# Performance work log

Measured on AMD Instinct MI355X. Metric: run time of the kernel, lower is better.

Reference implementation:

```python
import jax, jax.numpy as jnp
import numpy as np

B, S, H = 4, 2048, 2048
FFN, E, TOP_K = 5632, 8, 2

def setup_inputs() -> dict:
    key = jax.random.key(0)
    k1, k2, k3, k4, k5 = jax.random.split(key, 5)
    return {
        "hidden_states": jax.random.normal(k1, (B, S, H), dtype=jnp.float32),
        "wg": jax.random.normal(k2, (H, E), dtype=jnp.float32) * 0.02,
        "wg_ema": jnp.zeros((H, E), dtype=jnp.float32),
        "fc1_1": jax.random.normal(k3, (E, FFN, H), dtype=jnp.float32) * 0.02,
        "fc1_2": jax.random.normal(k4, (E, FFN, H), dtype=jnp.float32) * 0.02,
        "fc2": jax.random.normal(k5, (E, H, FFN), dtype=jnp.float32) * 0.02,
    }

def reference(hidden_states, wg, wg_ema, fc1_1, fc1_2, fc2):
    b, s, h = hidden_states.shape
    x = hidden_states.reshape(-1, h)  # [T, H]
    # Router: P6TopkCapGate mixes the live gate with its EMA 50/50.
    wg_running = 0.5 * (wg_ema + wg.astype(jnp.float32))
    router_logits = x.astype(jnp.float32) @ wg_running  # [T, E]
    probs = jax.nn.softmax(router_logits, axis=-1)
    top_vals, top_idx = jax.lax.top_k(probs, TOP_K)  # [T, K]
    routing_weights = (top_vals / top_vals.sum(axis=-1, keepdims=True)).astype(x.dtype)
    out = jnp.zeros_like(x)
    n_experts = fc1_1.shape[0]
    for e in range(n_experts):
        # combine weight per token for this expert (0 if not routed here)
        w_e = jnp.sum(routing_weights * (top_idx == e), axis=-1)  # [T]
        h1 = x @ fc1_1[e].T            # [T, FFN]
        h2 = x @ fc1_2[e].T            # [T, FFN]
        y = (jax.nn.silu(h1) * h2) @ fc2[e].T  # [T, H]
        out = out + w_e[:, None] * y
    return out.reshape(b, s, h), router_logits
```

## Files before the change

### kernel.cpp

```cpp
#include <hip/hip_runtime.h>
#include <stdint.h>

#define TT 8192
#define HD 2048
#define FFN 5632
#define NE 8
#define NPK 11264

typedef float f32x4 __attribute__((ext_vector_type(4)));
typedef _Float16 f16x8 __attribute__((ext_vector_type(8)));
typedef unsigned int u32;

#define OFF_WR    0ul
#define OFF_CNT   65536ul
#define OFF_LISTS 66048ul
#define OFF_TOKW  328192ul
#define OFF_ACT   1048576ul
#define OFF_XH    (OFF_ACT + 184549376ul)
#define OFF_WPK   (OFF_XH + 33554432ul)
#define OFF_W3H   OFF_WPK

__device__ __forceinline__ void gl_lds16(const void* g, void* s) {
  __builtin_amdgcn_global_load_lds((const __attribute__((address_space(1))) u32*)g,
                                   (__attribute__((address_space(3))) u32*)s, 16, 0, 0);
}

#define VM4() asm volatile("s_waitcnt vmcnt(4)" ::: "memory")
#define VM0() asm volatile("s_waitcnt vmcnt(0)" ::: "memory")

__device__ __forceinline__ f16x8 cvt8(f32x4 a, f32x4 b) {
  f16x8 r;
  r[0] = (_Float16)a[0]; r[1] = (_Float16)a[1]; r[2] = (_Float16)a[2]; r[3] = (_Float16)a[3];
  r[4] = (_Float16)b[0]; r[5] = (_Float16)b[1]; r[6] = (_Float16)b[2]; r[7] = (_Float16)b[3];
  return r;
}

__global__ __launch_bounds__(256) void k_cvt(const float* __restrict__ in,
                                             _Float16* __restrict__ out, long n8) {
  long i = (long)blockIdx.x * 256 + threadIdx.x;
  const long stride = (long)gridDim.x * 256;
  for (; i < n8; i += stride) {
    f32x4 a = ((const f32x4*)in)[i * 2];
    f32x4 b = ((const f32x4*)in)[i * 2 + 1];
    ((f16x8*)out)[i] = cvt8(a, b);
  }
}

__global__ __launch_bounds__(256) void k_cvtpack(const float* __restrict__ fc11,
                                                 const float* __restrict__ fc12,
                                                 _Float16* __restrict__ wpk) {
  const long total = (long)NE * NPK * 256;
  long i8 = (long)blockIdx.x * 256 + threadIdx.x;
  const long stride = (long)gridDim.x * 256;
  for (; i8 < total; i8 += stride) {
    int k8 = (int)(i8 & 255);
    long qe = i8 >> 8;
    int q = (int)(qe % NPK);
    int e = (int)(qe / NPK);
    int c = q & 255;
    int f = (q >> 8) * 128 + ((c >> 6) & 3) * 32 + ((c >> 4) & 1) * 16 + (c & 15);
    const float* src = ((c >> 5) & 1 ? fc12 : fc11) + ((size_t)e * FFN + f) * HD + k8 * 8;
    f32x4 a = *(const f32x4*)src;
    f32x4 b = *(const f32x4*)(src + 4);
    *(f16x8*)(wpk + qe * HD + (size_t)k8 * 8) = cvt8(a, b);
  }
}

__global__ __launch_bounds__(256) void k_prep(const float* __restrict__ wg,
                                              const float* __restrict__ wge,
                                              float* __restrict__ wr) {
  int i = blockIdx.x * 256 + threadIdx.x;
  if (i < HD * NE) wr[i] = 0.5f * (wge[i] + wg[i]);
}

__global__ __launch_bounds__(256) void k_router(const float* __restrict__ x,
                                                const float* __restrict__ wr,
                                                float* __restrict__ logits,
                                                float* __restrict__ tokw,
                                                int* __restrict__ lists,
                                                int* __restrict__ cnt,
                                                _Float16* __restrict__ xh) {
  const int t = blockIdx.x, tid = threadIdx.x;
  const float* xr = x + (size_t)t * HD;
  _Float16* xo = xh + (size_t)t * HD;
  float acc[NE];
#pragma unroll
  for (int e = 0; e < NE; ++e) acc[e] = 0.f;
  for (int h = tid; h < HD; h += 256) {
    float xv = xr[h];
    xo[h] = (_Float16)xv;
    const float* w = wr + h * NE;
#pragma unroll
    for (int e = 0; e < NE; ++e) acc[e] = fmaf(xv, w[e], acc[e]);
  }
#pragma unroll
  for (int e = 0; e < NE; ++e)
#pragma unroll
    for (int off = 32; off; off >>= 1)
      acc[e] += __shfl_xor(acc[e], off, 64);
  __shared__ float red[4][NE];
  int wv = tid >> 6;
  if ((tid & 63) == 0)
    for (int e = 0; e < NE; ++e) red[wv][e] = acc[e];
  __syncthreads();
  if (tid == 0) {
    float l[NE];
#pragma unroll
    for (int e = 0; e < NE; ++e) l[e] = red[0][e] + red[1][e] + red[2][e] + red[3][e];
#pragma unroll
    for (int e = 0; e < NE; ++e) logits[(size_t)t * NE + e] = l[e];
    int i0 = 0;
    for (int e = 1; e < NE; ++e) if (l[e] > l[i0]) i0 = e;
    int i1 = -1;
    for (int e = 0; e < NE; ++e) if (e != i0 && (i1 < 0 || l[e] > l[i1])) i1 = e;
    float p1 = __expf(l[i1] - l[i0]);
    float s = 1.f + p1;
    tokw[t * 2]     = 1.f / s;
    tokw[t * 2 + 1] = p1 / s;
    int q0 = atomicAdd(&cnt[i0], 1);
    lists[i0 * TT + q0] = t * 2;
    int q1 = atomicAdd(&cnt[i1], 1);
    lists[i1 * TT + q1] = t * 2 + 1;
  }
}

__global__ __launch_bounds__(512, 2) void k_ffn1(const _Float16* __restrict__ xh,
                                                 const _Float16* __restrict__ wpk,
                                                 const int* __restrict__ lists,
                                                 const int* __restrict__ cnt,
                                                 _Float16* __restrict__ act) {
  const int bid = blockIdx.x;
  const int xk = bid & 7;
  const int sq = bid >> 3;
  const int slot = sq / 88;
  const int within = sq - slot * 88;
  const int ct = within >> 1;
  const int rt_in = within & 1;
  const int e = slot & 7;
  const int r = ((xk - e) & 7) + ((slot >> 3) << 3);
  const int rt = r * 2 + rt_in;
  const int count = cnt[e];
  if (rt * 256 >= count) return;
  const int tid = threadIdx.x, lane = tid & 63, wv = tid >> 6;

  __shared__ __align__(16) _Float16 As[3][8192];
  __shared__ __align__(16) _Float16 Bs[3][8192];
  __shared__ int row_pair[256];

  if (tid < 256) {
    int rg = rt * 256 + tid;
    row_pair[tid] = (rg < count) ? lists[e * TT + rg] : -1;
  }
  __syncthreads();

  const int lr = lane >> 2;
  const int r0 = wv * 16 + lr;
  const int cp = (((lane & 3) ^ ((r0 >> 1) & 3))) * 8;
  const int pr0 = row_pair[r0], pr1 = row_pair[r0 + 128];
  const _Float16* gA0 = xh + (size_t)(pr0 >= 0 ? (pr0 >> 1) : 0) * HD + cp;
  const _Float16* gA1 = xh + (size_t)(pr1 >= 0 ? (pr1 >> 1) : 0) * HD + cp;
  const _Float16* gB0 = wpk + ((size_t)e * NPK + (size_t)ct * 256 + r0) * HD + cp;
  const _Float16* gB1 = gB0 + (size_t)128 * HD;

  auto stgA = [&](int b, int k0) {
    gl_lds16(gA0 + k0, &As[b][wv * 512]);
    gl_lds16(gA1 + k0, &As[b][4096 + wv * 512]);
  };
  auto stgB = [&](int b, int k0) {
    gl_lds16(gB0 + k0, &Bs[b][wv * 512]);
    gl_lds16(gB1 + k0, &Bs[b][4096 + wv * 512]);
  };

  const f32x4 z4 = {0.f, 0.f, 0.f, 0.f};
  f32x4 acc[8][4];
#pragma unroll
  for (int m = 0; m < 8; ++m)
#pragma unroll
    for (int n = 0; n < 4; ++n) acc[m][n] = z4;

  const int fr = lane & 15, kq = lane >> 4;
  const int wm = wv >> 2, wn = wv & 3;
  int aoff[8], boff[4];
#pragma unroll
  for (int m = 0; m < 8; ++m) {
    int R = wm * 128 + m * 16 + fr;
    aoff[m] = R * 32 + (kq ^ ((R >> 1) & 3)) * 8;
  }
#pragma unroll
  for (int n = 0; n < 4; ++n) {
    int R = wn * 64 + n * 16 + fr;
    boff[n] = R * 32 + (kq ^ ((R >> 1) & 3)) * 8;
  }

  stgA(0, 0); stgB(0, 0);
  stgA(1, 32); stgB(1, 32);
  VM4();
  __builtin_amdgcn_s_barrier();

  const int NS = HD / 32;
  for (int s = 0; s < NS; ++s) {
    const int b = s % 3;
    const int pb = (s + 2) % 3;
    f16x8 fa[8], fb[4];
#pragma unroll
    for (int m = 0; m < 8; ++m) fa[m] = *(const f16x8*)&As[b][aoff[m]];
#pragma unroll
    for (int n = 0; n < 4; ++n) fb[n] = *(const f16x8*)&Bs[b][boff[n]];
    if (s + 2 < NS) { stgA(pb, (s + 2) * 32); stgB(pb, (s + 2) * 32); }
    __builtin_amdgcn_s_setprio(1);
#pragma unroll
    for (int m = 0; m < 8; ++m)
#pragma unroll
      for (int n = 0; n < 4; ++n)
        acc[m][n] = __builtin_amdgcn_mfma_f32_16x16x32_f16(fa[m], fb[n], acc[m][n], 0, 0, 0);
    __builtin_amdgcn_s_setprio(0);
    if (s < NS - 2) { VM4(); }
    else if (s == NS - 2) { VM0(); }
    __builtin_amdgcn_s_barrier();
  }

  const int rbase = wm * 128 + kq * 4;
#pragma unroll
  for (int m = 0; m < 8; ++m) {
#pragma unroll
    for (int n = 0; n < 2; ++n) {
      const int f = ct * 128 + wn * 32 + n * 16 + fr;
#pragma unroll
      for (int j = 0; j < 4; ++j) {
        int rl = rbase + m * 16 + j;
        int pr = row_pair[rl];
        if (pr >= 0) {
          float h1 = acc[m][n][j], h2 = acc[m][n + 2][j];
          float sv = h1 / (1.f + __expf(-h1));
          act[(size_t)pr * FFN + f] = (_Float16)(sv * h2);
        }
      }
    }
  }
}

__global__ __launch_bounds__(256, 3) void k_ffn2(const _Float16* __restrict__ act,
                                                 const _Float16* __restrict__ w3h,
                                                 const int* __restrict__ lists,
                                                 const int* __restrict__ cnt,
                                                 const float* __restrict__ tokw,
                                                 float* __restrict__ out) {
  const int bid = blockIdx.x;
  const int xk = bid & 7;
  const int sq = bid >> 3;
  const int e = sq / 88;
  const int within = sq - e * 88;
  const int rt = within >> 1;
  const int ct = (((xk - e) & 7) << 1) + (within & 1);
  const int count = cnt[e];
  if (rt * 192 >= count) return;
  const int tid = threadIdx.x, lane = tid & 63, wv = tid >> 6;

  __shared__ __align__(16) _Float16 As[2][6144];
  __shared__ __align__(16) _Float16 Bs[2][4096];
  __shared__ int row_pair[192];
  __shared__ float row_w[192];

  if (tid < 192) {
    int rg = rt * 192 + tid;
    int pr = (rg < count) ? lists[e * TT + rg] : -1;
    row_pair[tid] = pr;
    row_w[tid] = (pr >= 0) ? tokw[pr] : 0.f;
  }
  __syncthreads();

  const int lr = lane >> 2;
  const int srowA = wv * 48 + lr;
  const int cpA = (lane & 3) ^ ((srowA >> 1) & 3);
  const int pA0 = row_pair[srowA], pA1 = row_pair[srowA + 16], pA2 = row_pair[srowA + 32];
  const _Float16* gA0 = act + (size_t)(pA0 >= 0 ? pA0 : 0) * FFN + cpA * 8;
  const _Float16* gA1 = act + (size_t)(pA1 >= 0 ? pA1 : 0) * FFN + cpA * 8;
  const _Float16* gA2 = act + (size_t)(pA2 >= 0 ? pA2 : 0) * FFN + cpA * 8;
  const int srowB = wv * 32 + lr;
  const int cpB = (lane & 3) ^ ((srowB >> 1) & 3);
  const _Float16* gB0 = w3h + ((size_t)e * HD + (size_t)ct * 128 + srowB) * FFN + cpB * 8;
  const _Float16* gB1 = gB0 + (size_t)16 * FFN;

  auto stage = [&](int sl, int k0) {
    gl_lds16(gA0 + k0, &As[sl][wv * 1536]);
    gl_lds16(gA1 + k0, &As[sl][wv * 1536 + 512]);
    gl_lds16(gA2 + k0, &As[sl][wv * 1536 + 1024]);
    gl_lds16(gB0 + k0, &Bs[sl][wv * 1024]);
    gl_lds16(gB1 + k0, &Bs[sl][wv * 1024 + 512]);
  };

  const f32x4 z4 = {0.f, 0.f, 0.f, 0.f};
  f32x4 acc[6][4];
#pragma unroll
  for (int m = 0; m < 6; ++m)
#pragma unroll
    for (int n = 0; n < 4; ++n) acc[m][n] = z4;

  const int fr = lane & 15, kq = lane >> 4;
  const int wrow = (wv >> 1) * 96, wcol = (wv & 1) * 64;
  int aoff[6], boff[4];
#pragma unroll
  for (int m = 0; m < 6; ++m) {
    int rr = wrow + m * 16 + fr;
    aoff[m] = rr * 32 + (kq ^ ((rr >> 1) & 3)) * 8;
  }
#pragma unroll
  for (int n = 0; n < 4; ++n) {
    int rr = wcol + n * 16 + fr;
    boff[n] = rr * 32 + (kq ^ ((rr >> 1) & 3)) * 8;
  }

  stage(0, 0);
  __syncthreads();

  const int NS = FFN / 32;
  for (int ks = 0; ks < NS; ++ks) {
    const int buf = ks & 1;
    if (ks + 1 < NS) stage(buf ^ 1, (ks + 1) * 32);
    f16x8 fa[6], fb[4];
#pragma unroll
    for (int m = 0; m < 6; ++m) fa[m] = *(const f16x8*)&As[buf][aoff[m]];
#pragma unroll
    for (int n = 0; n < 4; ++n) fb[n] = *(const f16x8*)&Bs[buf][boff[n]];
    __builtin_amdgcn_s_setprio(1);
#pragma unroll
    for (int m = 0; m < 6; ++m)
#pragma unroll
      for (int n = 0; n < 4; ++n)
        acc[m][n] = __builtin_amdgcn_mfma_f32_16x16x32_f16(fa[m], fb[n], acc[m][n], 0, 0, 0);
    __builtin_amdgcn_s_setprio(0);
    __syncthreads();
  }

  const int rbase = wrow + kq * 4;
#pragma unroll
  for (int m = 0; m < 6; ++m) {
#pragma unroll
    for (int n = 0; n < 4; ++n) {
      const int col = ct * 128 + wcol + n * 16 + fr;
#pragma unroll
      for (int j = 0; j < 4; ++j) {
        int rl = rbase + m * 16 + j;
        int pr = row_pair[rl];
        if (pr >= 0) {
          float v = acc[m][n][j] * row_w[rl];
          unsafeAtomicAdd(out + (size_t)(pr >> 1) * HD + col, v);
        }
      }
    }
  }
}

extern "C" void kernel_launch(void* const* d_in, const int* in_sizes, int n_in,
                              void* d_out, int out_size, void* d_ws, size_t ws_size,
                              hipStream_t stream) {
  (void)in_sizes; (void)n_in; (void)out_size; (void)ws_size;
  const float* x    = (const float*)d_in[0];
  const float* wg   = (const float*)d_in[1];
  const float* wge  = (const float*)d_in[2];
  const float* fc11 = (const float*)d_in[3];
  const float* fc12 = (const float*)d_in[4];
  const float* fc2  = (const float*)d_in[5];
  float* out    = (float*)d_out;
  float* logits = out + (size_t)TT * HD;

  char* ws = (char*)d_ws;
  float* wr      = (float*)(ws + OFF_WR);
  int*   cnt     = (int*)(ws + OFF_CNT);
  int*   lists   = (int*)(ws + OFF_LISTS);
  float* tokw    = (float*)(ws + OFF_TOKW);
  _Float16* act  = (_Float16*)(ws + OFF_ACT);
  _Float16* xh   = (_Float16*)(ws + OFF_XH);
  _Float16* wpk  = (_Float16*)(ws + OFF_WPK);
  _Float16* w3h  = (_Float16*)(ws + OFF_W3H);

  hipMemsetAsync(out, 0, (size_t)TT * HD * sizeof(float), stream);
  hipMemsetAsync(cnt, 0, NE * sizeof(int), stream);

  k_prep<<<dim3((HD * NE + 255) / 256), 256, 0, stream>>>(wg, wge, wr);
  k_router<<<dim3(TT), 256, 0, stream>>>(x, wr, logits, tokw, lists, cnt, xh);

  k_cvtpack<<<dim3(2048), 256, 0, stream>>>(fc11, fc12, wpk);

  k_ffn1<<<dim3(8 * 16 * 88), 512, 0, stream>>>(xh, wpk, lists, cnt, act);

  k_cvt<<<dim3(2048), 256, 0, stream>>>(fc2, w3h, (long)NE * HD * FFN / 8);

  k_ffn2<<<dim3(8 * 8 * 88), 256, 0, stream>>>(act, w3h, lists, cnt, tokw, out);
}
```

Baseline: 1.913 ms.

## Enlarge ffn2 tiles to 256x256 with 512 threads and triple-buffered LDS pipeline

The down-projection kernel moves from 192x128 tiles on 4 waves to 256x256 tiles on 8 waves. Each wave now computes an 8x4 block of MFMA tiles. Loading uses a three-stage LDS ring with explicit vmcnt waits and raw barriers, prefetching two k-steps ahead instead of one. The aim is more operand reuse per byte loaded and better hiding of global-to-LDS latency. The cost is much higher LDS use (about 96KB per block), which may cut occupancy, and coarser tiles that waste more work on ragged per-expert row counts.

```diff
diff --git a/kernel.cpp b/kernel.cpp
--- a/kernel.cpp
+++ b/kernel.cpp
@@ -239,7 +239,7 @@
   }
 }
 
-__global__ __launch_bounds__(256, 3) void k_ffn2(const _Float16* __restrict__ act,
+__global__ __launch_bounds__(512, 2) void k_ffn2(const _Float16* __restrict__ act,
                                                  const _Float16* __restrict__ w3h,
                                                  const int* __restrict__ lists,
                                                  const int* __restrict__ cnt,
@@ -248,21 +248,20 @@
   const int bid = blockIdx.x;
   const int xk = bid & 7;
   const int sq = bid >> 3;
-  const int e = sq / 88;
-  const int within = sq - e * 88;
-  const int rt = within >> 1;
-  const int ct = (((xk - e) & 7) << 1) + (within & 1);
+  const int e = sq >> 5;
+  const int rt = sq & 31;
+  const int ct = (xk - e) & 7;
   const int count = cnt[e];
-  if (rt * 192 >= count) return;
+  if (rt * 256 >= count) return;
   const int tid = threadIdx.x, lane = tid & 63, wv = tid >> 6;
 
-  __shared__ __align__(16) _Float16 As[2][6144];
-  __shared__ __align__(16) _Float16 Bs[2][4096];
-  __shared__ int row_pair[192];
-  __shared__ float row_w[192];
-
-  if (tid < 192) {
-    int rg = rt * 192 + tid;
+  __shared__ __align__(16) _Float16 As[3][8192];
+  __shared__ __align__(16) _Float16 Bs[3][8192];
+  __shared__ int row_pair[256];
+  __shared__ float row_w[256];
+
+  if (tid < 256) {
+    int rg = rt * 256 + tid;
     int pr = (rg < count) ? lists[e * TT + rg] : -1;
     row_pair[tid] = pr;
     row_w[tid] = (pr >= 0) ? tokw[pr] : 0.f;
@@ -270,74 +269,77 @@
   __syncthreads();
 
   const int lr = lane >> 2;
-  const int srowA = wv * 48 + lr;
-  const int cpA = (lane & 3) ^ ((srowA >> 1) & 3);
-  const int pA0 = row_pair[srowA], pA1 = row_pair[srowA + 16], pA2 = row_pair[srowA + 32];
-  const _Float16* gA0 = act + (size_t)(pA0 >= 0 ? pA0 : 0) * FFN + cpA * 8;
-  const _Float16* gA1 = act + (size_t)(pA1 >= 0 ? pA1 : 0) * FFN + cpA * 8;
-  const _Float16* gA2 = act + (size_t)(pA2 >= 0 ? pA2 : 0) * FFN + cpA * 8;
-  const int srowB = wv * 32 + lr;
-  const int cpB = (lane & 3) ^ ((srowB >> 1) & 3);
-  const _Float16* gB0 = w3h + ((size_t)e * HD + (size_t)ct * 128 + srowB) * FFN + cpB * 8;
-  const _Float16* gB1 = gB0 + (size_t)16 * FFN;
-
-  auto stage = [&](int sl, int k0) {
-    gl_lds16(gA0 + k0, &As[sl][wv * 1536]);
-    gl_lds16(gA1 + k0, &As[sl][wv * 1536 + 512]);
-    gl_lds16(gA2 + k0, &As[sl][wv * 1536 + 1024]);
-    gl_lds16(gB0 + k0, &Bs[sl][wv * 1024]);
-    gl_lds16(gB1 + k0, &Bs[sl][wv * 1024 + 512]);
+  const int r0 = wv * 16 + lr;
+  const int cp = (((lane & 3) ^ ((r0 >> 1) & 3))) * 8;
+  const int pr0 = row_pair[r0], pr1 = row_pair[r0 + 128];
+  const _Float16* gA0 = act + (size_t)(pr0 >= 0 ? pr0 : 0) * FFN + cp;
+  const _Float16* gA1 = act + (size_t)(pr1 >= 0 ? pr1 : 0) * FFN + cp;
+  const _Float16* gB0 = w3h + ((size_t)e * HD + (size_t)ct * 256 + r0) * FFN + cp;
+  const _Float16* gB1 = gB0 + (size_t)128 * FFN;
+
+  auto stgA = [&](int b, int k0) {
+    gl_lds16(gA0 + k0, &As[b][wv * 512]);
+    gl_lds16(gA1 + k0, &As[b][4096 + wv * 512]);
   };
+  auto stgB = [&](int b, int k0) {
+    gl_lds16(gB0 + k0, &Bs[b][wv * 512]);
+    gl_lds16(gB1 + k0, &Bs[b][4096 + wv * 512]);
+  };
 
   const f32x4 z4 = {0.f, 0.f, 0.f, 0.f};
-  f32x4 acc[6][4];
-#pragma unroll
-  for (int m = 0; m < 6; ++m)
+  f32x4 acc[8][4];
+#pragma unroll
+  for (int m = 0; m < 8; ++m)
 #pragma unroll
     for (int n = 0; n < 4; ++n) acc[m][n] = z4;
 
   const int fr = lane & 15, kq = lane >> 4;
-  const int wrow = (wv >> 1) * 96, wcol = (wv & 1) * 64;
-  int aoff[6], boff[4];
-#pragma unroll
-  for (int m = 0; m < 6; ++m) {
-    int rr = wrow + m * 16 + fr;
-    aoff[m] = rr * 32 + (kq ^ ((rr >> 1) & 3)) * 8;
+  const int wm = wv >> 2, wn = wv & 3;
+  int aoff[8], boff[4];
+#pragma unroll
+  for (int m = 0; m < 8; ++m) {
+    int R = wm * 128 + m * 16 + fr;
+    aoff[m] = R * 32 + (kq ^ ((R >> 1) & 3)) * 8;
   }
 #pragma unroll
   for (int n = 0; n < 4; ++n) {
-    int rr = wcol + n * 16 + fr;
-    boff[n] = rr * 32 + (kq ^ ((rr >> 1) & 3)) * 8;
-  }
-
-  stage(0, 0);
-  __syncthreads();
+    int R = wn * 64 + n * 16 + fr;
+    boff[n] = R * 32 + (kq ^ ((R >> 1) & 3)) * 8;
+  }
+
+  stgA(0, 0); stgB(0, 0);
+  stgA(1, 32); stgB(1, 32);
+  VM4();
+  __builtin_amdgcn_s_barrier();
 
   const int NS = FFN / 32;
-  for (int ks = 0; ks < NS; ++ks) {
-    const int buf = ks & 1;
-    if (ks + 1 < NS) stage(buf ^ 1, (ks + 1) * 32);
-    f16x8 fa[6], fb[4];
-#pragma unroll
-    for (int m = 0; m < 6; ++m) fa[m] = *(const f16x8*)&As[buf][aoff[m]];
-#pragma unroll
-    for (int n = 0; n < 4; ++n) fb[n] = *(const f16x8*)&Bs[buf][boff[n]];
+  for (int s = 0; s < NS; ++s) {
+    const int b = s % 3;
+    const int pb = (s + 2) % 3;
+    f16x8 fa[8], fb[4];
+#pragma unroll
+    for (int m = 0; m < 8; ++m) fa[m] = *(const f16x8*)&As[b][aoff[m]];
+#pragma unroll
+    for (int n = 0; n < 4; ++n) fb[n] = *(const f16x8*)&Bs[b][boff[n]];
+    if (s + 2 < NS) { stgA(pb, (s + 2) * 32); stgB(pb, (s + 2) * 32); }
     __builtin_amdgcn_s_setprio(1);
 #pragma unroll
-    for (int m = 0; m < 6; ++m)
+    for (int m = 0; m < 8; ++m)
 #pragma unroll
       for (int n = 0; n < 4; ++n)
         acc[m][n] = __builtin_amdgcn_mfma_f32_16x16x32_f16(fa[m], fb[n], acc[m][n], 0, 0, 0);
     __builtin_amdgcn_s_setprio(0);
-    __syncthreads();
-  }
-
-  const int rbase = wrow + kq * 4;
-#pragma unroll
-  for (int m = 0; m < 6; ++m) {
+    if (s < NS - 2) { VM4(); }
+    else if (s == NS - 2) { VM0(); }
+    __builtin_amdgcn_s_barrier();
+  }
+
+  const int rbase = wm * 128 + kq * 4;
+#pragma unroll
+  for (int m = 0; m < 8; ++m) {
 #pragma unroll
     for (int n = 0; n < 4; ++n) {
-      const int col = ct * 128 + wcol + n * 16 + fr;
+      const int col = ct * 256 + wn * 64 + n * 16 + fr;
 #pragma unroll
       for (int j = 0; j < 4; ++j) {
         int rl = rbase + m * 16 + j;
@@ -386,5 +388,5 @@
 
   k_cvt<<<dim3(2048), 256, 0, stream>>>(fc2, w3h, (long)NE * HD * FFN / 8);
 
-  k_ffn2<<<dim3(8 * 8 * 88), 256, 0, stream>>>(act, w3h, lists, cnt, tokw, out);
-}
+  k_ffn2<<<dim3(8 * 8 * 32), 512, 0, stream>>>(act, w3h, lists, cnt, tokw, out);
+}
```

After: 1.961 ms. +2.5%, slower.

## Fuse fc2 fp32-to-fp16 conversion into ffn2 B-tile loading and drop k_cvt

Applied to the files above, without the earlier changes.

Removes the separate k_cvt pass that converted all of fc2 to fp16 in workspace. k_ffn2 now loads fp32 fc2 rows into registers, converts them to fp16 and writes them to LDS after the MFMA block. This is software pipelined against the existing async A-tile loads. The block index mapping is also reordered so row tiles vary fastest within an (expert, column-half), letting consecutive blocks reuse the same fp32 weight tile in cache. This saves a full read and write of the expert weights, but each block now pulls twice the bytes for B, and the synchronous register loads add latency and register pressure.

```diff
diff --git a/kernel.cpp b/kernel.cpp
--- a/kernel.cpp
+++ b/kernel.cpp
@@ -18,7 +18,6 @@
 #define OFF_ACT   1048576ul
 #define OFF_XH    (OFF_ACT + 184549376ul)
 #define OFF_WPK   (OFF_XH + 33554432ul)
-#define OFF_W3H   OFF_WPK
 
 __device__ __forceinline__ void gl_lds16(const void* g, void* s) {
   __builtin_amdgcn_global_load_lds((const __attribute__((address_space(1))) u32*)g,
@@ -33,17 +32,6 @@
   r[0] = (_Float16)a[0]; r[1] = (_Float16)a[1]; r[2] = (_Float16)a[2]; r[3] = (_Float16)a[3];
   r[4] = (_Float16)b[0]; r[5] = (_Float16)b[1]; r[6] = (_Float16)b[2]; r[7] = (_Float16)b[3];
   return r;
-}
-
-__global__ __launch_bounds__(256) void k_cvt(const float* __restrict__ in,
-                                             _Float16* __restrict__ out, long n8) {
-  long i = (long)blockIdx.x * 256 + threadIdx.x;
-  const long stride = (long)gridDim.x * 256;
-  for (; i < n8; i += stride) {
-    f32x4 a = ((const f32x4*)in)[i * 2];
-    f32x4 b = ((const f32x4*)in)[i * 2 + 1];
-    ((f16x8*)out)[i] = cvt8(a, b);
-  }
 }
 
 __global__ __launch_bounds__(256) void k_cvtpack(const float* __restrict__ fc11,
@@ -240,7 +228,7 @@
 }
 
 __global__ __launch_bounds__(256, 3) void k_ffn2(const _Float16* __restrict__ act,
-                                                 const _Float16* __restrict__ w3h,
+                                                 const float* __restrict__ fc2,
                                                  const int* __restrict__ lists,
                                                  const int* __restrict__ cnt,
                                                  const float* __restrict__ tokw,
@@ -250,8 +238,9 @@
   const int sq = bid >> 3;
   const int e = sq / 88;
   const int within = sq - e * 88;
-  const int rt = within >> 1;
-  const int ct = (((xk - e) & 7) << 1) + (within & 1);
+  const int cph = within / 44;
+  const int rt = within - cph * 44;
+  const int ct = (((xk - e) & 7) << 1) + cph;
   const int count = cnt[e];
   if (rt * 192 >= count) return;
   const int tid = threadIdx.x, lane = tid & 63, wv = tid >> 6;
@@ -278,15 +267,23 @@
   const _Float16* gA2 = act + (size_t)(pA2 >= 0 ? pA2 : 0) * FFN + cpA * 8;
   const int srowB = wv * 32 + lr;
   const int cpB = (lane & 3) ^ ((srowB >> 1) & 3);
-  const _Float16* gB0 = w3h + ((size_t)e * HD + (size_t)ct * 128 + srowB) * FFN + cpB * 8;
-  const _Float16* gB1 = gB0 + (size_t)16 * FFN;
-
-  auto stage = [&](int sl, int k0) {
+  const float* pb0 = fc2 + ((size_t)e * HD + (size_t)ct * 128 + srowB) * FFN + cpB * 8;
+  const float* pb1 = pb0 + (size_t)16 * FFN;
+
+  auto stageA = [&](int sl, int k0) {
     gl_lds16(gA0 + k0, &As[sl][wv * 1536]);
     gl_lds16(gA1 + k0, &As[sl][wv * 1536 + 512]);
     gl_lds16(gA2 + k0, &As[sl][wv * 1536 + 1024]);
-    gl_lds16(gB0 + k0, &Bs[sl][wv * 1024]);
-    gl_lds16(gB1 + k0, &Bs[sl][wv * 1024 + 512]);
+  };
+
+  f32x4 b00, b01, b10, b11;
+  auto loadB = [&](int k0) {
+    b00 = *(const f32x4*)(pb0 + k0); b01 = *(const f32x4*)(pb0 + k0 + 4);
+    b10 = *(const f32x4*)(pb1 + k0); b11 = *(const f32x4*)(pb1 + k0 + 4);
+  };
+  auto writeB = [&](int sl) {
+    *(f16x8*)&Bs[sl][wv * 1024 + lane * 8] = cvt8(b00, b01);
+    *(f16x8*)&Bs[sl][wv * 1024 + 512 + lane * 8] = cvt8(b10, b11);
   };
 
   const f32x4 z4 = {0.f, 0.f, 0.f, 0.f};
@@ -310,13 +307,18 @@
     boff[n] = rr * 32 + (kq ^ ((rr >> 1) & 3)) * 8;
   }
 
-  stage(0, 0);
+  loadB(0);
+  stageA(0, 0);
+  writeB(0);
   __syncthreads();
 
   const int NS = FFN / 32;
   for (int ks = 0; ks < NS; ++ks) {
     const int buf = ks & 1;
-    if (ks + 1 < NS) stage(buf ^ 1, (ks + 1) * 32);
+    if (ks + 1 < NS) {
+      loadB((ks + 1) * 32);
+      stageA(buf ^ 1, (ks + 1) * 32);
+    }
     f16x8 fa[6], fb[4];
 #pragma unroll
     for (int m = 0; m < 6; ++m) fa[m] = *(const f16x8*)&As[buf][aoff[m]];
@@ -329,6 +331,7 @@
       for (int n = 0; n < 4; ++n)
         acc[m][n] = __builtin_amdgcn_mfma_f32_16x16x32_f16(fa[m], fb[n], acc[m][n], 0, 0, 0);
     __builtin_amdgcn_s_setprio(0);
+    if (ks + 1 < NS) writeB(buf ^ 1);
     __syncthreads();
   }
 
@@ -372,7 +375,6 @@
   _Float16* act  = (_Float16*)(ws + OFF_ACT);
   _Float16* xh   = (_Float16*)(ws + OFF_XH);
   _Float16* wpk  = (_Float16*)(ws + OFF_WPK);
-  _Float16* w3h  = (_Float16*)(ws + OFF_W3H);
 
   hipMemsetAsync(out, 0, (size_t)TT * HD * sizeof(float), stream);
   hipMemsetAsync(cnt, 0, NE * sizeof(int), stream);
@@ -384,7 +386,5 @@
 
   k_ffn1<<<dim3(8 * 16 * 88), 512, 0, stream>>>(xh, wpk, lists, cnt, act);
 
-  k_cvt<<<dim3(2048), 256, 0, stream>>>(fc2, w3h, (long)NE * HD * FFN / 8);
-
-  k_ffn2<<<dim3(8 * 8 * 88), 256, 0, stream>>>(act, w3h, lists, cnt, tokw, out);
-}
+  k_ffn2<<<dim3(8 * 8 * 88), 256, 0, stream>>>(act, fc2, lists, cnt, tokw, out);
+}
```

Result: slower. 1.951 ms (+2.0%).

## Load expert weight fragments directly into registers instead of staging through LDS

Applied to the files above, without the earlier changes.

The gate/up GEMM kernel no longer stages the B (weight) tile through shared memory. Each wave loads its own B fragments from global memory straight into registers, double-buffered across k-steps, and only the A tile still goes through LDS, now with two buffers instead of three. This cuts LDS traffic and footprint, which may allow higher occupancy. In exchange, B fragments are reloaded by both wm wave rows (duplicate global reads), the row loads are no longer coalesced 16B reads through global_load_lds, the pipeline is shallower, and the loop uses full __syncthreads rather than vmcnt-tuned waits.

```diff
diff --git a/kernel.cpp b/kernel.cpp
--- a/kernel.cpp
+++ b/kernel.cpp
@@ -24,9 +24,6 @@
   __builtin_amdgcn_global_load_lds((const __attribute__((address_space(1))) u32*)g,
                                    (__attribute__((address_space(3))) u32*)s, 16, 0, 0);
 }
-
-#define VM4() asm volatile("s_waitcnt vmcnt(4)" ::: "memory")
-#define VM0() asm volatile("s_waitcnt vmcnt(0)" ::: "memory")
 
 __device__ __forceinline__ f16x8 cvt8(f32x4 a, f32x4 b) {
   f16x8 r;
@@ -143,8 +140,7 @@
   if (rt * 256 >= count) return;
   const int tid = threadIdx.x, lane = tid & 63, wv = tid >> 6;
 
-  __shared__ __align__(16) _Float16 As[3][8192];
-  __shared__ __align__(16) _Float16 Bs[3][8192];
+  __shared__ __align__(16) _Float16 As[2][8192];
   __shared__ int row_pair[256];
 
   if (tid < 256) {
@@ -159,17 +155,11 @@
   const int pr0 = row_pair[r0], pr1 = row_pair[r0 + 128];
   const _Float16* gA0 = xh + (size_t)(pr0 >= 0 ? (pr0 >> 1) : 0) * HD + cp;
   const _Float16* gA1 = xh + (size_t)(pr1 >= 0 ? (pr1 >> 1) : 0) * HD + cp;
-  const _Float16* gB0 = wpk + ((size_t)e * NPK + (size_t)ct * 256 + r0) * HD + cp;
-  const _Float16* gB1 = gB0 + (size_t)128 * HD;
 
   auto stgA = [&](int b, int k0) {
     gl_lds16(gA0 + k0, &As[b][wv * 512]);
     gl_lds16(gA1 + k0, &As[b][4096 + wv * 512]);
   };
-  auto stgB = [&](int b, int k0) {
-    gl_lds16(gB0 + k0, &Bs[b][wv * 512]);
-    gl_lds16(gB1 + k0, &Bs[b][4096 + wv * 512]);
-  };
 
   const f32x4 z4 = {0.f, 0.f, 0.f, 0.f};
   f32x4 acc[8][4];
@@ -180,44 +170,53 @@
 
   const int fr = lane & 15, kq = lane >> 4;
   const int wm = wv >> 2, wn = wv & 3;
-  int aoff[8], boff[4];
+  int aoff[8];
 #pragma unroll
   for (int m = 0; m < 8; ++m) {
     int R = wm * 128 + m * 16 + fr;
     aoff[m] = R * 32 + (kq ^ ((R >> 1) & 3)) * 8;
   }
+  const _Float16* gb[4];
 #pragma unroll
   for (int n = 0; n < 4; ++n) {
-    int R = wn * 64 + n * 16 + fr;
-    boff[n] = R * 32 + (kq ^ ((R >> 1) & 3)) * 8;
-  }
-
-  stgA(0, 0); stgB(0, 0);
-  stgA(1, 32); stgB(1, 32);
-  VM4();
-  __builtin_amdgcn_s_barrier();
+    int grow = ct * 256 + wn * 64 + n * 16 + fr;
+    gb[n] = wpk + ((size_t)e * NPK + grow) * HD + kq * 8;
+  }
+
+  f16x8 fb0[4], fb1[4];
+#define BLOAD(FB, S)                                                        \
+  {                                                                         \
+    _Pragma("unroll") for (int n = 0; n < 4; ++n)                           \
+        FB[n] = *(const f16x8*)(gb[n] + (S) * 32);                          \
+  }
+
+  stgA(0, 0);
+  BLOAD(fb0, 0);
+  __syncthreads();
 
   const int NS = HD / 32;
-  for (int s = 0; s < NS; ++s) {
-    const int b = s % 3;
-    const int pb = (s + 2) % 3;
-    f16x8 fa[8], fb[4];
-#pragma unroll
-    for (int m = 0; m < 8; ++m) fa[m] = *(const f16x8*)&As[b][aoff[m]];
-#pragma unroll
-    for (int n = 0; n < 4; ++n) fb[n] = *(const f16x8*)&Bs[b][boff[n]];
-    if (s + 2 < NS) { stgA(pb, (s + 2) * 32); stgB(pb, (s + 2) * 32); }
-    __builtin_amdgcn_s_setprio(1);
-#pragma unroll
-    for (int m = 0; m < 8; ++m)
-#pragma unroll
-      for (int n = 0; n < 4; ++n)
-        acc[m][n] = __builtin_amdgcn_mfma_f32_16x16x32_f16(fa[m], fb[n], acc[m][n], 0, 0, 0);
-    __builtin_amdgcn_s_setprio(0);
-    if (s < NS - 2) { VM4(); }
-    else if (s == NS - 2) { VM0(); }
-    __builtin_amdgcn_s_barrier();
-  }
+#define STEP(S, CUR, NXT)                                                   \
+  {                                                                         \
+    const int buf = (S) & 1;                                                \
+    if ((S) + 1 < NS) { stgA(buf ^ 1, ((S) + 1) * 32); BLOAD(NXT, (S) + 1); } \
+    f16x8 fa[8];                                                            \
+    _Pragma("unroll") for (int m = 0; m < 8; ++m)                           \
+        fa[m] = *(const f16x8*)&As[buf][aoff[m]];                           \
+    __builtin_amdgcn_s_setprio(1);                                          \
+    _Pragma("unroll") for (int m = 0; m < 8; ++m)                           \
+      _Pragma("unroll") for (int n = 0; n < 4; ++n)                         \
+          acc[m][n] = __builtin_amdgcn_mfma_f32_16x16x32_f16(               \
+              fa[m], CUR[n], acc[m][n], 0, 0, 0);                           \
+    __builtin_amdgcn_s_setprio(0);                                          \
+    __syncthreads();                                                        \
+  }
+
+  for (int s = 0; s < NS; s += 2) {
+    STEP(s, fb0, fb1);
+    STEP(s + 1, fb1, fb0);
+  }
+#undef STEP
+#undef BLOAD
 
   const int rbase = wm * 128 + kq * 4;
 #pragma unroll
```

Result: slower. 2.454 ms (+28.3%).
